# Optimization experiments

Measured on AMD Instinct MI355X. Metric: run time of the kernel, lower is better.

## Reference

```python
import jax, jax.numpy as jnp
import numpy as np

B, N, D, H = 4096, 64, 32, 64

def setup_inputs() -> dict:
    key = jax.random.key(0)
    ks = jax.random.split(key, 10)
    s = lambda fan_in: 1.0 / np.sqrt(fan_in)
    return {
        "joint_features": jax.random.normal(ks[0], (B, N, D), jnp.float32),
        "Wm1": jax.random.uniform(ks[1], (2 * D, H), jnp.float32, -s(2 * D), s(2 * D)),
        "bm1": jax.random.uniform(ks[2], (H,), jnp.float32, -s(2 * D), s(2 * D)),
        "Wm2": jax.random.uniform(ks[3], (H, D), jnp.float32, -s(H), s(H)),
        "bm2": jax.random.uniform(ks[4], (D,), jnp.float32, -s(H), s(H)),
        "Wu1": jax.random.uniform(ks[5], (2 * D, H), jnp.float32, -s(2 * D), s(2 * D)),
        "bu1": jax.random.uniform(ks[6], (H,), jnp.float32, -s(2 * D), s(2 * D)),
        "Wu2": jax.random.uniform(ks[7], (H, D), jnp.float32, -s(H), s(H)),
        "bu2": jax.random.uniform(ks[8], (D,), jnp.float32, -s(H), s(H)),
        "residual_weight": jnp.float32(0.5),
        "num_joints": N,
    }

def reference(joint_features, Wm1, bm1, Wm2, bm2, Wu1, bu1, Wu2, bu2, residual_weight, num_joints):
    n = num_joints
    # chain topology: directed edges (i->i+1) and (i+1->i); dst receives message
    dst = jnp.concatenate([jnp.arange(n - 1), jnp.arange(1, n)])  # [E]
    src = jnp.concatenate([jnp.arange(1, n), jnp.arange(n - 1)])  # [E]
    # edge gather + concat: [B, E, 2D]
    edge_in = jnp.concatenate([joint_features[:, dst], joint_features[:, src]], axis=-1)
    # message MLP (ReLU after both layers, per original Sequential)
    msg = jax.nn.relu(jax.nn.relu(edge_in @ Wm1 + bm1) @ Wm2 + bm2)  # [B, E, D]
    # scatter-add messages to destination nodes
    messages = jnp.zeros_like(joint_features).at[:, dst].add(msg)  # [B, N, D]
    # per-node update MLP on concat(feature, message)
    upd_in = jnp.concatenate([joint_features, messages], axis=-1)  # [B, N, 2D]
    updated = jax.nn.relu(upd_in @ Wu1 + bu1) @ Wu2 + bu2  # [B, N, D]
    return residual_weight * updated + (1.0 - residual_weight) * joint_features
```

## Files before the change

### kernel.cpp

```cpp
#include <hip/hip_runtime.h>
#include <hip/hip_bf16.h>


typedef __bf16 bf16x8 __attribute__((ext_vector_type(8)));
typedef float  f32x4  __attribute__((ext_vector_type(4)));
typedef unsigned short u16;

#define NBATCH 8
#define NBI 2
#define ITERS (NBATCH / NBI)
#define HS  72
#define MBS 40

__device__ __forceinline__ u16 f2b(float f) { return __builtin_bit_cast(u16, (__bf16)f); }
__device__ __forceinline__ f32x4 MFMA(bf16x8 a, bf16x8 b, f32x4 c) {
    return __builtin_amdgcn_mfma_f32_16x16x32_bf16(a, b, c, 0, 0, 0);
}
__device__ __forceinline__ bf16x8 pack8(float4 a, float4 b) {
    bf16x8 r = {(__bf16)a.x, (__bf16)a.y, (__bf16)a.z, (__bf16)a.w,
                (__bf16)b.x, (__bf16)b.y, (__bf16)b.z, (__bf16)b.w};
    return r;
}

__global__ __launch_bounds__(256, 2)
void agn_mfma(const float* __restrict__ x, const float* __restrict__ Wm1,
              const float* __restrict__ bm1, const float* __restrict__ Wm2,
              const float* __restrict__ bm2, const float* __restrict__ Wu1,
              const float* __restrict__ bu1, const float* __restrict__ Wu2,
              const float* __restrict__ bu2, const float* __restrict__ rw_p,
              float* __restrict__ out)
{
    __shared__ __align__(16) u16 sH[256 * HS];
    __shared__ __align__(16) u16 sMB[256 * MBS];

    const int t = threadIdx.x;
    const int w = t >> 6;
    const int lane = t & 63;
    const int ln = lane & 15;
    const int q  = lane >> 4;

    bf16x8 B1a[4], B1b[4], B2[2][2], B3[2][4], B4[2][2];
#pragma unroll
    for (int nt = 0; nt < 4; ++nt)
#pragma unroll
        for (int j = 0; j < 8; ++j) {
            B1a[nt][j] = (__bf16)Wm1[(q * 8 + j) * 64 + nt * 16 + ln];
            B1b[nt][j] = (__bf16)Wm1[(32 + q * 8 + j) * 64 + nt * 16 + ln];
        }
#pragma unroll
    for (int s = 0; s < 2; ++s)
#pragma unroll
        for (int nt = 0; nt < 2; ++nt)
#pragma unroll
            for (int j = 0; j < 8; ++j)
                B2[s][nt][j] = (__bf16)Wm2[(s * 32 + q * 8 + j) * 32 + nt * 16 + ln];
#pragma unroll
    for (int s = 0; s < 2; ++s)
#pragma unroll
        for (int nt = 0; nt < 4; ++nt)
#pragma unroll
            for (int j = 0; j < 8; ++j)
                B3[s][nt][j] = (__bf16)Wu1[(s * 32 + q * 8 + j) * 64 + nt * 16 + ln];
#pragma unroll
    for (int s = 0; s < 2; ++s)
#pragma unroll
        for (int nt = 0; nt < 2; ++nt)
#pragma unroll
            for (int j = 0; j < 8; ++j)
                B4[s][nt][j] = (__bf16)Wu2[(s * 32 + q * 8 + j) * 32 + nt * 16 + ln];

    float bm1v[4], bu1v[4], bm2v[2], bu2v[2];
#pragma unroll
    for (int nt = 0; nt < 4; ++nt) { bm1v[nt] = bm1[nt * 16 + ln]; bu1v[nt] = bu1[nt * 16 + ln]; }
#pragma unroll
    for (int nt = 0; nt < 2; ++nt) { bm2v[nt] = bm2[nt * 16 + ln]; bu2v[nt] = bu2[nt * 16 + ln]; }
    const float rw = rw_p[0];
    const float om = 1.f - rw;

    const size_t base = (size_t)blockIdx.x * (NBATCH * 64 * 32);

    for (int it = 0; it < ITERS; ++it) {
        const float* xit = x + base + (size_t)it * (NBI * 64 * 32);
        float*       oit = out + base + (size_t)it * (NBI * 64 * 32);

        {
            float4 xd[4][2], xsv[4][2];
#pragma unroll
            for (int m = 0; m < 4; ++m) {
                const int mt = 4 * w + m;
                const int erow = mt * 16 + ln;
                const int bb = erow >> 7;
                int e = erow & 127;
                if (e >= 126) e = 0;
                const int dst  = (e < 63) ? e : e - 62;
                const int srcn = (e < 63) ? e + 1 : e - 63;
                const float* pd = xit + ((bb << 6) + dst) * 32 + q * 8;
                const float* ps = xit + ((bb << 6) + srcn) * 32 + q * 8;
                xd[m][0] = *(const float4*)pd;  xd[m][1] = *(const float4*)(pd + 4);
                xsv[m][0] = *(const float4*)ps; xsv[m][1] = *(const float4*)(ps + 4);
            }
#pragma unroll
            for (int m = 0; m < 4; ++m) {
                const int mt = 4 * w + m;
                bf16x8 Ad = pack8(xd[m][0], xd[m][1]);
                bf16x8 As = pack8(xsv[m][0], xsv[m][1]);
#pragma unroll
                for (int nt = 0; nt < 4; ++nt) {
                    f32x4 acc = {0.f, 0.f, 0.f, 0.f};
                    acc = MFMA(Ad, B1a[nt], acc);
                    acc = MFMA(As, B1b[nt], acc);
                    const int rb = mt * 16 + q * 4;
                    const int c  = nt * 16 + ln;
#pragma unroll
                    for (int r = 0; r < 4; ++r)
                        sH[(rb + r) * HS + c] = f2b(fmaxf(acc[r] + bm1v[nt], 0.f));
                }
            }
        }
        __syncthreads();

#pragma unroll
        for (int m = 0; m < 4; ++m) {
            const int mt = 4 * w + m;
            const int row = mt * 16 + ln;
            bf16x8 A0 = __builtin_bit_cast(bf16x8, *(const uint4*)&sH[row * HS + q * 8]);
            bf16x8 A1 = __builtin_bit_cast(bf16x8, *(const uint4*)&sH[row * HS + 32 + q * 8]);
#pragma unroll
            for (int nt = 0; nt < 2; ++nt) {
                f32x4 acc = {0.f, 0.f, 0.f, 0.f};
                acc = MFMA(A0, B2[0][nt], acc);
                acc = MFMA(A1, B2[1][nt], acc);
                const int rb = mt * 16 + q * 4;
                const int c  = nt * 16 + ln;
#pragma unroll
                for (int r = 0; r < 4; ++r)
                    sMB[(rb + r) * MBS + c] = f2b(fmaxf(acc[r] + bm2v[nt], 0.f));
            }
        }
        __syncthreads();

#pragma unroll
        for (int m = 0; m < 2; ++m) {
            const int mt = 2 * w + m;
            const int row = mt * 16 + ln;
            const int bb = row >> 6;
            const int i2 = row & 63;
            const float* p = xit + row * 32 + q * 8;
            float4 a0 = *(const float4*)p;
            float4 a1 = *(const float4*)(p + 4);
            bf16x8 A0 = pack8(a0, a1);
            float mv[8] = {0.f, 0.f, 0.f, 0.f, 0.f, 0.f, 0.f, 0.f};
            if (i2 < 63) {
                uint4 u = *(const uint4*)&sMB[((bb << 7) + i2) * MBS + q * 8];
                const unsigned* pu = (const unsigned*)&u;
#pragma unroll
                for (int h = 0; h < 4; ++h) {
                    mv[2 * h]     += __uint_as_float(pu[h] << 16);
                    mv[2 * h + 1] += __uint_as_float(pu[h] & 0xFFFF0000u);
                }
            }
            if (i2 > 0) {
                uint4 u = *(const uint4*)&sMB[((bb << 7) + 62 + i2) * MBS + q * 8];
                const unsigned* pu = (const unsigned*)&u;
#pragma unroll
                for (int h = 0; h < 4; ++h) {
                    mv[2 * h]     += __uint_as_float(pu[h] << 16);
                    mv[2 * h + 1] += __uint_as_float(pu[h] & 0xFFFF0000u);
                }
            }
            bf16x8 A1;
#pragma unroll
            for (int j = 0; j < 8; ++j) A1[j] = (__bf16)mv[j];
#pragma unroll
            for (int nt = 0; nt < 4; ++nt) {
                f32x4 acc = {0.f, 0.f, 0.f, 0.f};
                acc = MFMA(A0, B3[0][nt], acc);
                acc = MFMA(A1, B3[1][nt], acc);
                const int rb = mt * 16 + q * 4;
                const int c  = nt * 16 + ln;
#pragma unroll
                for (int r = 0; r < 4; ++r)
                    sH[(rb + r) * HS + c] = f2b(fmaxf(acc[r] + bu1v[nt], 0.f));
            }
        }
        __syncthreads();

#pragma unroll
        for (int m = 0; m < 2; ++m) {
            const int mt = 2 * w + m;
            const int arow = mt * 16 + ln;
            bf16x8 A0 = __builtin_bit_cast(bf16x8, *(const uint4*)&sH[arow * HS + q * 8]);
            bf16x8 A1 = __builtin_bit_cast(bf16x8, *(const uint4*)&sH[arow * HS + 32 + q * 8]);
#pragma unroll
            for (int nt = 0; nt < 2; ++nt) {
                f32x4 acc = {0.f, 0.f, 0.f, 0.f};
                acc = MFMA(A0, B4[0][nt], acc);
                acc = MFMA(A1, B4[1][nt], acc);
                const int rb = mt * 16 + q * 4;
                const int c  = nt * 16 + ln;
#pragma unroll
                for (int r = 0; r < 4; ++r) {
                    const int off = (rb + r) * 32 + c;
                    oit[off] = rw * (acc[r] + bu2v[nt]) + om * xit[off];
                }
            }
        }
        __syncthreads();
    }
}

extern "C" void kernel_launch(void* const* d_in, const int* in_sizes, int n_in,
                              void* d_out, int out_size, void* d_ws, size_t ws_size,
                              hipStream_t stream) {
    const float* x   = (const float*)d_in[0];
    const float* Wm1 = (const float*)d_in[1];
    const float* bm1 = (const float*)d_in[2];
    const float* Wm2 = (const float*)d_in[3];
    const float* bm2 = (const float*)d_in[4];
    const float* Wu1 = (const float*)d_in[5];
    const float* bu1 = (const float*)d_in[6];
    const float* Wu2 = (const float*)d_in[7];
    const float* bu2 = (const float*)d_in[8];
    const float* rw  = (const float*)d_in[9];
    float* out = (float*)d_out;

    const int B = in_sizes[0] / (64 * 32);
    agn_mfma<<<B / NBATCH, 256, 0, stream>>>(x, Wm1, bm1, Wm2, bm2, Wu1, bu1, Wu2, bu2, rw, out);
}
```

Before: 121.4 us.

## Transpose MFMA operands to write packed rows and drop block barriers

After: 124.2 us. +2.3%, slower.

```diff
diff --git a/kernel.cpp b/kernel.cpp
--- a/kernel.cpp
+++ b/kernel.cpp
@@ -20,6 +20,22 @@
     bf16x8 r = {(__bf16)a.x, (__bf16)a.y, (__bf16)a.z, (__bf16)a.w,
                 (__bf16)b.x, (__bf16)b.y, (__bf16)b.z, (__bf16)b.w};
     return r;
+}
+__device__ __forceinline__ uint2 relu_pack4(f32x4 acc, f32x4 bias) {
+    uint2 o;
+    o.x = (unsigned)f2b(fmaxf(acc[0] + bias[0], 0.f)) |
+          ((unsigned)f2b(fmaxf(acc[1] + bias[1], 0.f)) << 16);
+    o.y = (unsigned)f2b(fmaxf(acc[2] + bias[2], 0.f)) |
+          ((unsigned)f2b(fmaxf(acc[3] + bias[3], 0.f)) << 16);
+    return o;
+}
+__device__ __forceinline__ void wave_lds_fence() {
+    asm volatile("s_waitcnt lgkmcnt(0)" ::: "memory");
+}
+__device__ __forceinline__ void barrier_lds() {
+    asm volatile("s_waitcnt lgkmcnt(0)" ::: "memory");
+    __builtin_amdgcn_s_barrier();
+    asm volatile("" ::: "memory");
 }
 
 __global__ __launch_bounds__(256, 2)
@@ -69,11 +85,22 @@
             for (int j = 0; j < 8; ++j)
                 B4[s][nt][j] = (__bf16)Wu2[(s * 32 + q * 8 + j) * 32 + nt * 16 + ln];
 
-    float bm1v[4], bu1v[4], bm2v[2], bu2v[2];
-#pragma unroll
-    for (int nt = 0; nt < 4; ++nt) { bm1v[nt] = bm1[nt * 16 + ln]; bu1v[nt] = bu1[nt * 16 + ln]; }
-#pragma unroll
-    for (int nt = 0; nt < 2; ++nt) { bm2v[nt] = bm2[nt * 16 + ln]; bu2v[nt] = bu2[nt * 16 + ln]; }
+    f32x4 bm1s[4], bu1s[4], bm2s[2];
+#pragma unroll
+    for (int ht = 0; ht < 4; ++ht)
+#pragma unroll
+        for (int r = 0; r < 4; ++r) {
+            bm1s[ht][r] = bm1[ht * 16 + q * 4 + r];
+            bu1s[ht][r] = bu1[ht * 16 + q * 4 + r];
+        }
+#pragma unroll
+    for (int s = 0; s < 2; ++s)
+#pragma unroll
+        for (int r = 0; r < 4; ++r)
+            bm2s[s][r] = bm2[s * 16 + q * 4 + r];
+    float bu2v[2];
+#pragma unroll
+    for (int nt = 0; nt < 2; ++nt) bu2v[nt] = bu2[nt * 16 + ln];
     const float rw = rw_p[0];
     const float om = 1.f - rw;
 
@@ -87,8 +114,8 @@
             float4 xd[4][2], xsv[4][2];
 #pragma unroll
             for (int m = 0; m < 4; ++m) {
-                const int mt = 4 * w + m;
-                const int erow = mt * 16 + ln;
+                const int et = 4 * w + m;
+                const int erow = et * 16 + ln;
                 const int bb = erow >> 7;
                 int e = erow & 127;
                 if (e >= 126) e = 0;
@@ -101,48 +128,39 @@
             }
 #pragma unroll
             for (int m = 0; m < 4; ++m) {
-                const int mt = 4 * w + m;
+                const int erow = (4 * w + m) * 16 + ln;
                 bf16x8 Ad = pack8(xd[m][0], xd[m][1]);
                 bf16x8 As = pack8(xsv[m][0], xsv[m][1]);
-#pragma unroll
-                for (int nt = 0; nt < 4; ++nt) {
+                u16* rowp = &sH[erow * HS];
+#pragma unroll
+                for (int ht = 0; ht < 4; ++ht) {
                     f32x4 acc = {0.f, 0.f, 0.f, 0.f};
-                    acc = MFMA(Ad, B1a[nt], acc);
-                    acc = MFMA(As, B1b[nt], acc);
-                    const int rb = mt * 16 + q * 4;
-                    const int c  = nt * 16 + ln;
-#pragma unroll
-                    for (int r = 0; r < 4; ++r)
-                        sH[(rb + r) * HS + c] = f2b(fmaxf(acc[r] + bm1v[nt], 0.f));
-                }
-            }
-        }
-        __syncthreads();
+                    acc = MFMA(B1a[ht], Ad, acc);
+                    acc = MFMA(B1b[ht], As, acc);
+                    *(uint2*)&rowp[ht * 16 + q * 4] = relu_pack4(acc, bm1s[ht]);
+                }
+            }
+        }
+        wave_lds_fence();
 
 #pragma unroll
         for (int m = 0; m < 4; ++m) {
-            const int mt = 4 * w + m;
-            const int row = mt * 16 + ln;
+            const int row = (4 * w + m) * 16 + ln;
             bf16x8 A0 = __builtin_bit_cast(bf16x8, *(const uint4*)&sH[row * HS + q * 8]);
             bf16x8 A1 = __builtin_bit_cast(bf16x8, *(const uint4*)&sH[row * HS + 32 + q * 8]);
 #pragma unroll
-            for (int nt = 0; nt < 2; ++nt) {
+            for (int s = 0; s < 2; ++s) {
                 f32x4 acc = {0.f, 0.f, 0.f, 0.f};
-                acc = MFMA(A0, B2[0][nt], acc);
-                acc = MFMA(A1, B2[1][nt], acc);
-                const int rb = mt * 16 + q * 4;
-                const int c  = nt * 16 + ln;
-#pragma unroll
-                for (int r = 0; r < 4; ++r)
-                    sMB[(rb + r) * MBS + c] = f2b(fmaxf(acc[r] + bm2v[nt], 0.f));
-            }
-        }
-        __syncthreads();
+                acc = MFMA(B2[0][s], A0, acc);
+                acc = MFMA(B2[1][s], A1, acc);
+                *(uint2*)&sMB[row * MBS + s * 16 + q * 4] = relu_pack4(acc, bm2s[s]);
+            }
+        }
+        barrier_lds();
 
 #pragma unroll
         for (int m = 0; m < 2; ++m) {
-            const int mt = 2 * w + m;
-            const int row = mt * 16 + ln;
+            const int row = (2 * w + m) * 16 + ln;
             const int bb = row >> 6;
             const int i2 = row & 63;
             const float* p = xit + row * 32 + q * 8;
@@ -172,18 +190,14 @@
 #pragma unroll
             for (int j = 0; j < 8; ++j) A1[j] = (__bf16)mv[j];
 #pragma unroll
-            for (int nt = 0; nt < 4; ++nt) {
+            for (int ht = 0; ht < 4; ++ht) {
                 f32x4 acc = {0.f, 0.f, 0.f, 0.f};
-                acc = MFMA(A0, B3[0][nt], acc);
-                acc = MFMA(A1, B3[1][nt], acc);
-                const int rb = mt * 16 + q * 4;
-                const int c  = nt * 16 + ln;
-#pragma unroll
-                for (int r = 0; r < 4; ++r)
-                    sH[(rb + r) * HS + c] = f2b(fmaxf(acc[r] + bu1v[nt], 0.f));
-            }
-        }
-        __syncthreads();
+                acc = MFMA(B3[0][ht], A0, acc);
+                acc = MFMA(B3[1][ht], A1, acc);
+                *(uint2*)&sH[row * HS + ht * 16 + q * 4] = relu_pack4(acc, bu1s[ht]);
+            }
+        }
+        wave_lds_fence();
 
 #pragma unroll
         for (int m = 0; m < 2; ++m) {
@@ -205,7 +219,7 @@
                 }
             }
         }
-        __syncthreads();
+        barrier_lds();
     }
 }
 
```
